# Performance work log

Hardware: AMD Instinct MI355X
Metric: run time of the kernel (lower is better)

Reference implementation:

```python
import jax, jax.numpy as jnp
import numpy as np

DIM = 384
NH = 16
HD = DIM // NH          # 24
HID = DIM * 4           # titan/cms hidden
RD = 2 * (HD // 3 // 2) # 8 rope channels per axis (d/h/w), 3*RD == HD


def _ln(x, scale, bias):
    m = x.mean(-1, keepdims=True)
    v = ((x - m) ** 2).mean(-1, keepdims=True)
    return (x - m) * jax.lax.rsqrt(v + 1e-5) * scale + bias


def _mlp(x, w1, b1, w2, b2):
    # TitanMemory / CMS level: Linear -> GELU -> Linear (titan_layers=2)
    h = jax.nn.gelu(x @ w1 + b1, approximate=False)
    return h @ w2 + b2


def _rotate(x, pos):
    # rotate_queries_or_keys: interleaved rotary. x: [B,nh,N,d], pos: [N]
    d = x.shape[-1]
    inv_freq = 1.0 / (10000.0 ** (jnp.arange(0, d, 2, dtype=jnp.float32) / d))
    ang = pos[:, None] * inv_freq[None, :]              # [N, d/2]
    sin, cos = jnp.sin(ang), jnp.cos(ang)
    x1, x2 = x[..., 0::2], x[..., 1::2]
    y1 = x1 * cos - x2 * sin
    y2 = x1 * sin + x2 * cos
    return jnp.stack([y1, y2], axis=-1).reshape(x.shape)


def _rope3d(q, T, H, W):
    # 3D RoPE on frame tokens (action_tokens=0): time / height / width axes
    B, N, D = q.shape
    qh = q.reshape(B, N, NH, HD).transpose(0, 2, 1, 3)   # [B,nh,N,hd]
    ids = jnp.arange(T * H * W)
    tpos = (ids // (H * W)).astype(jnp.float32)
    hpos = ((ids % (H * W)) // W).astype(jnp.float32)
    wpos = (ids % W).astype(jnp.float32)
    qd = _rotate(qh[..., :RD], tpos)
    qhh = _rotate(qh[..., RD:2 * RD], hpos)
    qww = _rotate(qh[..., 2 * RD:3 * RD], wpos)
    out = jnp.concatenate([qd, qhh, qww], axis=-1)
    return out.transpose(0, 2, 1, 3).reshape(B, N, D)


def setup_inputs() -> dict:
    key = jax.random.key(0)
    ks = jax.random.split(key, 8)
    B, T, H, W = 8, 8, 16, 16
    N = T * H * W
    p = lambda k, sh: jax.random.normal(k, sh, jnp.float32) * 0.02
    return {
        "x": jax.random.normal(ks[0], (B, N, DIM), jnp.float32),
        "norm1_scale": jnp.ones((DIM,), jnp.float32),
        "norm1_bias": jnp.zeros((DIM,), jnp.float32),
        "norm2_scale": jnp.ones((DIM,), jnp.float32),
        "norm2_bias": jnp.zeros((DIM,), jnp.float32),
        "q_w": p(ks[1], (DIM, DIM)),
        # stacked Titan memories: [M_k, M_v, M_eta, M_alpha, M_memory]
        "titan_w1": p(ks[2], (5, DIM, HID)),
        "titan_b1": jnp.zeros((5, HID), jnp.float32),
        "titan_w2": p(ks[3], (5, HID, DIM)),
        "titan_b2": jnp.zeros((5, DIM), jnp.float32),
        "out_w": p(ks[4], (DIM, DIM)),
        "out_b": jnp.zeros((DIM,), jnp.float32),
        # CMS levels: [fast, medium, slow]
        "cms_w1": p(ks[5], (3, DIM, HID)),
        "cms_b1": jnp.zeros((3, HID), jnp.float32),
        "cms_w2": p(ks[6], (3, HID, DIM)),
        "cms_b2": jnp.zeros((3, DIM), jnp.float32),
        "T": T, "H": H, "W": W, "action_tokens": 0,
    }


def reference(x, norm1_scale, norm1_bias, norm2_scale, norm2_bias, q_w,
              titan_w1, titan_b1, titan_w2, titan_b2, out_w, out_b,
              cms_w1, cms_b1, cms_w2, cms_b2, T, H, W, action_tokens):
    # Phase A: self-modifying Titan (eval path: retrieval only)
    y = _ln(x, norm1_scale, norm1_bias)
    q = y @ q_w                                  # static query projection (Eq. 76)
    q = _rope3d(q, T, H, W)                      # 3D RoPE (action_tokens == 0)
    out = _mlp(q, titan_w1[4], titan_b1[4], titan_w2[4], titan_b2[4])  # M_memory(q)
    out = out @ out_w + out_b                    # out_proj
    x = x + out                                  # residual (drop_path = identity)
    # Phase B: CMS multi-frequency MLP cascade
    y = _ln(x, norm2_scale, norm2_bias)
    cms = sum(_mlp(y, cms_w1[i], cms_b1[i], cms_w2[i], cms_b2[i]) for i in range(3))
    return x + cms
```

## Files before the change

kernel.cpp:

```cpp
#include <hip/hip_runtime.h>
#include <math.h>

typedef unsigned short u16;
typedef unsigned int u32;
typedef __attribute__((ext_vector_type(8))) short short8;
typedef __attribute__((ext_vector_type(4))) float f32x4;

#define DIM 384
#define HID 1536

static __device__ __forceinline__ float bf2f(u32 b){ return __uint_as_float(b << 16); }
static __device__ __forceinline__ u16 f2bf(float f){
  u32 u = __float_as_uint(f);
  u32 r = (u + 0x7fffu + ((u >> 16) & 1u)) >> 16;
  return (u16)r;
}
static __device__ __forceinline__ float gelu_fast(float v){
  float u = v * fmaf(0.0713548162726f, v * v, 1.59576912161f);
  float e = __builtin_amdgcn_exp2f(-1.44269504089f * u);
  return v * __builtin_amdgcn_rcpf(1.0f + e);
}
static __device__ __forceinline__ void gload_lds16(const u16* g, u16* l){
  __builtin_amdgcn_global_load_lds(
      (__attribute__((address_space(1))) void*)(void*)const_cast<u16*>(g),
      (__attribute__((address_space(3))) void*)(void*)l, 16, 0, 0);
}
template<int N> static __device__ __forceinline__ void vm_wait(){
  if constexpr (N == 0)      asm volatile("s_waitcnt vmcnt(0)" ::: "memory");
  else if constexpr (N == 4) asm volatile("s_waitcnt vmcnt(4)" ::: "memory");
  else if constexpr (N == 5) asm volatile("s_waitcnt vmcnt(5)" ::: "memory");
  else if constexpr (N == 6) asm volatile("s_waitcnt vmcnt(6)" ::: "memory");
  else                       asm volatile("s_waitcnt vmcnt(0)" ::: "memory");
}
static __device__ __forceinline__ void barrier_raw(){
  asm volatile("s_barrier" ::: "memory");
}
static __device__ __forceinline__ void lgkm_wait0(){
  asm volatile("s_waitcnt lgkmcnt(0)" ::: "memory");
}

__global__ __launch_bounds__(256) void ln_kernel(const float* __restrict__ x,
    const float* __restrict__ sc, const float* __restrict__ bi, u16* __restrict__ y){
  int lane = threadIdx.x & 63;
  int row = blockIdx.x * 4 + (threadIdx.x >> 6);
  const float* xr = x + (size_t)row * DIM;
  float v[6];
  float s = 0.f, sq = 0.f;
#pragma unroll
  for (int i = 0; i < 6; ++i){
    float f = xr[lane + 64*i];
    v[i] = f; s += f; sq += f*f;
  }
#pragma unroll
  for (int o = 1; o < 64; o <<= 1){ s += __shfl_xor(s, o); sq += __shfl_xor(sq, o); }
  float mean = s * (1.0f/DIM);
  float var = sq * (1.0f/DIM) - mean*mean;
  float inv = rsqrtf(var + 1e-5f);
  u16* yr = y + (size_t)row * DIM;
#pragma unroll
  for (int i = 0; i < 6; ++i){
    int c = lane + 64*i;
    yr[c] = f2bf((v[i] - mean) * inv * sc[c] + bi[c]);
  }
}

__global__ __launch_bounds__(256) void rope_kernel(u16* __restrict__ q,
    const int* __restrict__ Tp, const int* __restrict__ Hp, const int* __restrict__ Wp,
    int Mtok){
  int idx = blockIdx.x * 256 + threadIdx.x;
  int tok = idx / 192;
  if (tok >= Mtok) return;
  int p = idx - tok * 192;
  int H = *Hp, W = *Wp, T = *Tp;
  int HW = H * W;
  int Ns = T * HW;
  int n = tok % Ns;
  int head = p / 12;
  int pp = p - head * 12;
  int s = pp >> 2, f = pp & 3;
  float pos;
  if (s == 0)      pos = (float)(n / HW);
  else if (s == 1) pos = (float)((n / W) % H);
  else             pos = (float)(n % W);
  const float LOG2_10000 = 13.28771237954945f;
  float inv = __builtin_amdgcn_exp2f(-0.25f * (float)f * LOG2_10000);
  float ang = pos * inv;
  float sn = __sinf(ang), cs = __cosf(ang);
  size_t base = (size_t)tok * DIM + head * 24 + s * 8 + 2 * f;
  u32 u = *(u32*)(q + base);
  float x1 = bf2f(u & 0xffffu), x2 = bf2f(u >> 16);
  float y1 = x1 * cs - x2 * sn;
  float y2 = x1 * sn + x2 * cs;
  *(u32*)(q + base) = (u32)f2bf(y1) | ((u32)f2bf(y2) << 16);
}

template<int R, int C>
__global__ __launch_bounds__(256) void transpose_kernel(
    const float* __restrict__ s0, const float* __restrict__ s1,
    const float* __restrict__ s2, const float* __restrict__ s3,
    u16* __restrict__ d0, u16* __restrict__ d1, u16* __restrict__ d2, u16* __restrict__ d3,
    int dstStride){
  const float* src = (blockIdx.z == 0) ? s0 : (blockIdx.z == 1) ? s1 : (blockIdx.z == 2) ? s2 : s3;
  u16* dst         = (blockIdx.z == 0) ? d0 : (blockIdx.z == 1) ? d1 : (blockIdx.z == 2) ? d2 : d3;
  __shared__ u16 t[32][33];
  int tx = threadIdx.x & 31, ty = threadIdx.x >> 5;
  int r0 = blockIdx.y * 32, c0 = blockIdx.x * 32;
#pragma unroll
  for (int i = 0; i < 4; ++i)
    t[ty + 8*i][tx] = f2bf(src[(size_t)(r0 + ty + 8*i) * C + c0 + tx]);
  __syncthreads();
#pragma unroll
  for (int i = 0; i < 4; ++i)
    dst[(size_t)(c0 + ty + 8*i) * dstStride + r0 + tx] = t[tx][ty + 8*i];
}

__global__ void bias3_kernel(const float* __restrict__ b, float* __restrict__ o){
  int n = threadIdx.x;
  o[n] = b[n] + b[384 + n] + b[768 + n];
}

enum { E_NONE = 0, E_BIAS = 1, E_RES_F32 = 3, E_FINAL = 5 };

template<int BM, int N, int K, int EPI>
__global__ __launch_bounds__(256) void gemm_kernel(
    const u16* __restrict__ A, const u16* __restrict__ Bt,
    void* __restrict__ Cv, const float* __restrict__ bias,
    const float* __restrict__ res, float* __restrict__ accbuf){
  constexpr int BN = 128, BK = 64;
  constexpr int MT = BM / 32, NT = 4;
  constexpr int AIT = BM / 32, BIT = 4;
  __shared__ __align__(16) u16 As[BM * BK];
  __shared__ __align__(16) u16 Bs[BN * BK];
  const int tid = threadIdx.x;
  const int lane = tid & 63;
  const int wv = tid >> 6;
  const int wm = (wv >> 1) * (BM / 2);
  const int wn = (wv & 1) * 64;
  const int quad = lane >> 4;
  const int l16 = lane & 15;
  const int rsw = l16 & 7;
  const size_t m0 = (size_t)blockIdx.x * BM;
  const int n0 = blockIdx.y * BN;
  const int srow = lane >> 3;
  const int scol = ((lane & 7) ^ srow) * 8;

  f32x4 acc[MT][NT];
  const f32x4 zero = {0.f, 0.f, 0.f, 0.f};
#pragma unroll
  for (int mt = 0; mt < MT; ++mt)
#pragma unroll
    for (int nt = 0; nt < NT; ++nt) acc[mt][nt] = zero;

  for (int kt = 0; kt < K; kt += BK){
#pragma unroll
    for (int i = 0; i < AIT; ++i){
      int seg = i * 4 + wv;
      gload_lds16(A + (m0 + (size_t)(seg * 8 + srow)) * K + kt + scol, As + seg * 512);
    }
#pragma unroll
    for (int i = 0; i < BIT; ++i){
      int seg = i * 4 + wv;
      gload_lds16(Bt + (size_t)(n0 + seg * 8 + srow) * K + kt + scol, Bs + seg * 512);
    }
    __syncthreads();
#pragma unroll
    for (int kk = 0; kk < 2; ++kk){
      short8 af[MT], bfr[NT];
#pragma unroll
      for (int mt = 0; mt < MT; ++mt)
        af[mt] = *(const short8*)(As + (wm + mt*16 + l16) * BK + (((kk*4 + quad) ^ rsw) << 3));
#pragma unroll
      for (int nt = 0; nt < NT; ++nt)
        bfr[nt] = *(const short8*)(Bs + (wn + nt*16 + l16) * BK + (((kk*4 + quad) ^ rsw) << 3));
#pragma unroll
      for (int mt = 0; mt < MT; ++mt)
#pragma unroll
        for (int nt = 0; nt < NT; ++nt)
          acc[mt][nt] = __builtin_amdgcn_mfma_f32_16x16x32_bf16(af[mt], bfr[nt], acc[mt][nt], 0, 0, 0);
    }
    __syncthreads();
  }

#pragma unroll
  for (int mt = 0; mt < MT; ++mt){
#pragma unroll
    for (int nt = 0; nt < NT; ++nt){
      int ncol = n0 + wn + nt*16 + l16;
      float bv = (EPI != E_NONE) ? bias[ncol] : 0.f;
      size_t mbase = m0 + wm + mt*16 + quad*4;
#pragma unroll
      for (int r = 0; r < 4; ++r){
        size_t off = (mbase + r) * N + ncol;
        float vv = acc[mt][nt][r];
        if      (EPI == E_NONE)      ((u16*)Cv)[off] = f2bf(vv);
        else if (EPI == E_BIAS)      ((u16*)Cv)[off] = f2bf(vv + bv);
        else          accbuf[off] = vv + bv + res[off];
      }
    }
  }
}

template<int HIDT, int NCH, int EPI>
__global__ __launch_bounds__(512, 2) void fused_mlp4_kernel(
    const u16* __restrict__ A, const u16* __restrict__ W1t, const u16* __restrict__ W2t,
    const float* __restrict__ b1, const float* __restrict__ b2,
    const float* __restrict__ accbuf, void* __restrict__ outp){
  __shared__ __align__(16) u16 As[6 * 64 * 64];
  __shared__ __align__(16) u16 ring[2][256 * 64];
  __shared__ __align__(16) u16 Hs[4 * 64 * 64];

  const int tid  = threadIdx.x;
  const int lane = tid & 63;
  const int wv   = tid >> 6;
  const int quad = lane >> 4;
  const int l16  = lane & 15;
  const int rsw  = l16 & 7;
  const size_t m0 = (size_t)blockIdx.x * 64;
  const int srow = lane >> 3;
  const int scol = ((lane & 7) ^ srow) * 8;
  const int uwm = (wv & 1) * 32;
  const int pan = wv >> 1;
  const int dwn = wv * 48;

  auto stage_up = [&](int hc, int kt, u16* buf){
#pragma unroll
    for (int i = 0; i < 4; ++i){
      int rg = i * 8 + wv;
      gload_lds16(W1t + ((size_t)hc + rg * 8 + srow) * 384 + kt * 64 + scol,
                  buf + rg * 512);
    }
  };

#pragma unroll
  for (int i = 0; i < 6; ++i)
    gload_lds16(A + (m0 + (size_t)(wv * 8 + srow)) * 384 + i * 64 + scol,
                As + (i * 8 + wv) * 512);
  stage_up(0, 0, ring[0]);

  f32x4 cacc[4][3];
  const f32x4 zero = {0.f, 0.f, 0.f, 0.f};
#pragma unroll
  for (int mt = 0; mt < 4; ++mt)
#pragma unroll
    for (int nt = 0; nt < 3; ++nt) cacc[mt][nt] = zero;

  for (int c = 0; c < NCH; ++c){
    const int hc = c * 256;
    f32x4 hacc[2][4];
#pragma unroll
    for (int mt = 0; mt < 2; ++mt)
#pragma unroll
      for (int nt = 0; nt < 4; ++nt) hacc[mt][nt] = zero;

#pragma unroll
    for (int kt = 0; kt < 6; ++kt){
      if (kt < 5)           { stage_up(hc, kt + 1, ring[(kt + 1) & 1]); vm_wait<4>(); }
      else if (c + 1 < NCH) { stage_up(hc + 256, 0, ring[0]);           vm_wait<4>(); }
      else                  { vm_wait<0>(); }
      barrier_raw();
      const u16* buf = ring[kt & 1];
#pragma unroll
      for (int kk = 0; kk < 2; ++kk){
        short8 af[2], bfr[4];
#pragma unroll
        for (int mt = 0; mt < 2; ++mt)
          af[mt] = *(const short8*)(As + kt*4096 + (uwm + mt*16 + l16) * 64 + (((kk*4 + quad) ^ rsw) << 3));
#pragma unroll
        for (int nt = 0; nt < 4; ++nt)
          bfr[nt] = *(const short8*)(buf + (pan*64 + nt*16 + l16) * 64 + (((kk*4 + quad) ^ rsw) << 3));
#pragma unroll
        for (int mt = 0; mt < 2; ++mt)
#pragma unroll
          for (int nt = 0; nt < 4; ++nt)
            hacc[mt][nt] = __builtin_amdgcn_mfma_f32_16x16x32_bf16(af[mt], bfr[nt], hacc[mt][nt], 0, 0, 0);
      }
      barrier_raw();
    }

#pragma unroll
    for (int nt = 0; nt < 4; ++nt){
      int pc = nt*16 + l16;
      float bv = b1[hc + pan*64 + pc];
      u16* hp = Hs + pan*4096;
#pragma unroll
      for (int mt = 0; mt < 2; ++mt){
#pragma unroll
        for (int r = 0; r < 4; ++r){
          int row = uwm + mt*16 + quad*4 + r;
          hp[row*64 + (((pc >> 3) ^ (row & 7)) << 3) + (pc & 7)] = f2bf(gelu_fast(hacc[mt][nt][r] + bv));
        }
      }
    }
    lgkm_wait0();
    barrier_raw();

    short8 wb[2][3];
#pragma unroll
    for (int nt = 0; nt < 3; ++nt)
      wb[0][nt] = *(const short8*)(W2t + (size_t)(dwn + nt*16 + l16) * HIDT + hc + quad*8);
#pragma unroll
    for (int s = 0; s < 8; ++s){
      if (s < 7){
        int off = ((s+1) >> 1) * 64 + (((s+1) & 1) * 4 + quad) * 8;
#pragma unroll
        for (int nt = 0; nt < 3; ++nt)
          wb[(s+1) & 1][nt] = *(const short8*)(W2t + (size_t)(dwn + nt*16 + l16) * HIDT + hc + off);
      }
      int dt = s >> 1, kk = s & 1;
      short8 af[4];
#pragma unroll
      for (int mt = 0; mt < 4; ++mt)
        af[mt] = *(const short8*)(Hs + dt*4096 + (mt*16 + l16) * 64 + (((kk*4 + quad) ^ rsw) << 3));
#pragma unroll
      for (int mt = 0; mt < 4; ++mt)
#pragma unroll
        for (int nt = 0; nt < 3; ++nt)
          cacc[mt][nt] = __builtin_amdgcn_mfma_f32_16x16x32_bf16(af[mt], wb[s & 1][nt], cacc[mt][nt], 0, 0, 0);
    }
  }

#pragma unroll
  for (int nt = 0; nt < 3; ++nt){
    int col = dwn + nt*16 + l16;
    float bv = b2[col];
#pragma unroll
    for (int mt = 0; mt < 4; ++mt){
      size_t mbase = m0 + mt*16 + quad*4;
#pragma unroll
      for (int r = 0; r < 4; ++r){
        size_t off = (mbase + r) * DIM + col;
        float vv = cacc[mt][nt][r] + bv;
        if (EPI == E_BIAS) ((u16*)outp)[off] = f2bf(vv);
        else  ((float*)outp)[off] = accbuf[off] + vv;
      }
    }
  }
}

extern "C" void kernel_launch(void* const* d_in, const int* in_sizes, int n_in,
                              void* d_out, int out_size, void* d_ws, size_t ws_size,
                              hipStream_t stream) {
  const int W11 = DIM * HID;
  const float* x   = (const float*)d_in[0];
  const float* n1s = (const float*)d_in[1];
  const float* n1b = (const float*)d_in[2];
  const float* n2s = (const float*)d_in[3];
  const float* n2b = (const float*)d_in[4];
  const float* qw  = (const float*)d_in[5];
  const float* tw1 = (const float*)d_in[6] + 4 * W11;
  const float* tb1 = (const float*)d_in[7] + 4 * HID;
  const float* tw2 = (const float*)d_in[8] + 4 * W11;
  const float* tb2 = (const float*)d_in[9] + 4 * DIM;
  const float* ow  = (const float*)d_in[10];
  const float* ob  = (const float*)d_in[11];
  const float* cw1 = (const float*)d_in[12];
  const float* cb1 = (const float*)d_in[13];
  const float* cw2 = (const float*)d_in[14];
  const float* cb2 = (const float*)d_in[15];
  const int* Tp = (const int*)d_in[16];
  const int* Hp = (const int*)d_in[17];
  const int* Wp = (const int*)d_in[18];
  const int M = in_sizes[0] / DIM;

  char* ws = (char*)d_ws;
  if (ws_size < 22611456u) return;
  u16*  y    = (u16*) (ws + 0);
  u16*  qwT  = (u16*) (ws + 12582912);
  u16*  owT  = (u16*) (ws + 12877824);
  u16*  w1T  = (u16*) (ws + 13172736);
  u16*  w2T  = (u16*) (ws + 14352384);
  u16*  cw1T = (u16*) (ws + 15532032);
  u16*  cw2T = (u16*) (ws + 19070976);
  float* cb2s = (float*)(ws + 22609920);
  u16*  qb   = (u16*)d_out;

  transpose_kernel<384,384><<<dim3(12,12,2),256,0,stream>>>(
      qw, ow, qw, qw, qwT, owT, qwT, qwT, 384);
  transpose_kernel<384,1536><<<dim3(48,12,4),256,0,stream>>>(
      tw1, cw1, cw1 + W11, cw1 + 2*W11, w1T, cw1T, cw1T + W11, cw1T + 2*W11, 384);
  transpose_kernel<1536,384><<<dim3(12,48,1),256,0,stream>>>(
      tw2, tw2, tw2, tw2, w2T, w2T, w2T, w2T, 1536);
  transpose_kernel<1536,384><<<dim3(12,48,3),256,0,stream>>>(
      cw2, cw2 + W11, cw2 + 2*W11, cw2, cw2T, cw2T + 1536, cw2T + 3072, cw2T, 4608);
  bias3_kernel<<<1,384,0,stream>>>(cb2, cb2s);

  ln_kernel<<<M/4,256,0,stream>>>(x, n1s, n1b, y);
  gemm_kernel<64,384,384,E_NONE><<<dim3(M/64,3),256,0,stream>>>(y, qwT, qb, nullptr, nullptr, nullptr);
  rope_kernel<<<(M*192)/256,256,0,stream>>>(qb, Tp, Hp, Wp, M);
  fused_mlp4_kernel<1536,6,E_BIAS><<<M/64,512,0,stream>>>(
      qb, w1T, w2T, tb1, tb2, nullptr, y);
  gemm_kernel<64,384,384,E_RES_F32><<<dim3(M/64,3),256,0,stream>>>(
      y, owT, nullptr, ob, x, (float*)d_out);
  ln_kernel<<<M/4,256,0,stream>>>((const float*)d_out, n2s, n2b, y);
  fused_mlp4_kernel<4608,18,E_FINAL><<<M/64,512,0,stream>>>(
      y, cw1T, cw2T, cb1, cb2s, (const float*)d_out, d_out);
}
```

Baseline: 450.8 us.

## Halve fused MLP row tile to 32 and drop double-buffered W1 staging

The fused MLP kernel now processes 32 rows per block instead of 64, doubling the grid and shrinking LDS so more blocks can be resident (launch bounds raised to 4 blocks per CU). The double-buffered W1 ring with manual vmcnt waits is replaced by a single staging buffer loaded each k-step and guarded by __syncthreads. The aim is more occupancy and parallelism, but each block now streams the same weights for half as many rows, doubling weight traffic. Weight-load latency is also no longer overlapped with compute inside a block.

```diff
diff --git a/kernel.cpp b/kernel.cpp
--- a/kernel.cpp
+++ b/kernel.cpp
@@ -24,19 +24,6 @@
   __builtin_amdgcn_global_load_lds(
       (__attribute__((address_space(1))) void*)(void*)const_cast<u16*>(g),
       (__attribute__((address_space(3))) void*)(void*)l, 16, 0, 0);
-}
-template<int N> static __device__ __forceinline__ void vm_wait(){
-  if constexpr (N == 0)      asm volatile("s_waitcnt vmcnt(0)" ::: "memory");
-  else if constexpr (N == 4) asm volatile("s_waitcnt vmcnt(4)" ::: "memory");
-  else if constexpr (N == 5) asm volatile("s_waitcnt vmcnt(5)" ::: "memory");
-  else if constexpr (N == 6) asm volatile("s_waitcnt vmcnt(6)" ::: "memory");
-  else                       asm volatile("s_waitcnt vmcnt(0)" ::: "memory");
-}
-static __device__ __forceinline__ void barrier_raw(){
-  asm volatile("s_barrier" ::: "memory");
-}
-static __device__ __forceinline__ void lgkm_wait0(){
-  asm volatile("s_waitcnt lgkmcnt(0)" ::: "memory");
 }
 
 __global__ __launch_bounds__(256) void ln_kernel(const float* __restrict__ x,
@@ -201,13 +188,13 @@
 }
 
 template<int HIDT, int NCH, int EPI>
-__global__ __launch_bounds__(512, 2) void fused_mlp4_kernel(
+__global__ __launch_bounds__(512, 4) void fused_mlp5_kernel(
     const u16* __restrict__ A, const u16* __restrict__ W1t, const u16* __restrict__ W2t,
     const float* __restrict__ b1, const float* __restrict__ b2,
     const float* __restrict__ accbuf, void* __restrict__ outp){
-  __shared__ __align__(16) u16 As[6 * 64 * 64];
-  __shared__ __align__(16) u16 ring[2][256 * 64];
-  __shared__ __align__(16) u16 Hs[4 * 64 * 64];
+  __shared__ __align__(16) u16 As[6 * 32 * 64];
+  __shared__ __align__(16) u16 WB[256 * 64];
+  __shared__ __align__(16) u16 Hs[4 * 32 * 64];
 
   const int tid  = threadIdx.x;
   const int lane = tid & 63;
@@ -215,84 +202,77 @@
   const int quad = lane >> 4;
   const int l16  = lane & 15;
   const int rsw  = l16 & 7;
-  const size_t m0 = (size_t)blockIdx.x * 64;
+  const size_t m0 = (size_t)blockIdx.x * 32;
   const int srow = lane >> 3;
   const int scol = ((lane & 7) ^ srow) * 8;
-  const int uwm = (wv & 1) * 32;
-  const int pan = wv >> 1;
+  const int pan = wv;
   const int dwn = wv * 48;
 
-  auto stage_up = [&](int hc, int kt, u16* buf){
-#pragma unroll
-    for (int i = 0; i < 4; ++i){
-      int rg = i * 8 + wv;
-      gload_lds16(W1t + ((size_t)hc + rg * 8 + srow) * 384 + kt * 64 + scol,
-                  buf + rg * 512);
-    }
-  };
-
-#pragma unroll
-  for (int i = 0; i < 6; ++i)
-    gload_lds16(A + (m0 + (size_t)(wv * 8 + srow)) * 384 + i * 64 + scol,
-                As + (i * 8 + wv) * 512);
-  stage_up(0, 0, ring[0]);
-
-  f32x4 cacc[4][3];
+#pragma unroll
+  for (int i = 0; i < 3; ++i){
+    int g = wv * 3 + i;
+    gload_lds16(A + (m0 + (size_t)((g & 3) * 8 + srow)) * 384 + (g >> 2) * 64 + scol,
+                As + g * 512);
+  }
+
+  f32x4 cacc[2][3];
   const f32x4 zero = {0.f, 0.f, 0.f, 0.f};
 #pragma unroll
-  for (int mt = 0; mt < 4; ++mt)
+  for (int mt = 0; mt < 2; ++mt)
 #pragma unroll
     for (int nt = 0; nt < 3; ++nt) cacc[mt][nt] = zero;
 
   for (int c = 0; c < NCH; ++c){
     const int hc = c * 256;
-    f32x4 hacc[2][4];
+    f32x4 hacc[2][2];
 #pragma unroll
     for (int mt = 0; mt < 2; ++mt)
 #pragma unroll
-      for (int nt = 0; nt < 4; ++nt) hacc[mt][nt] = zero;
-
-#pragma unroll
+      for (int nt = 0; nt < 2; ++nt) hacc[mt][nt] = zero;
+
     for (int kt = 0; kt < 6; ++kt){
-      if (kt < 5)           { stage_up(hc, kt + 1, ring[(kt + 1) & 1]); vm_wait<4>(); }
-      else if (c + 1 < NCH) { stage_up(hc + 256, 0, ring[0]);           vm_wait<4>(); }
-      else                  { vm_wait<0>(); }
-      barrier_raw();
-      const u16* buf = ring[kt & 1];
+#pragma unroll
+      for (int i = 0; i < 4; ++i){
+        int g = i * 8 + wv;
+        gload_lds16(W1t + ((size_t)hc + g * 8 + srow) * 384 + kt * 64 + scol,
+                    WB + g * 512);
+      }
+      __syncthreads();
 #pragma unroll
       for (int kk = 0; kk < 2; ++kk){
-        short8 af[2], bfr[4];
+        short8 af[2], bfr[2];
 #pragma unroll
         for (int mt = 0; mt < 2; ++mt)
-          af[mt] = *(const short8*)(As + kt*4096 + (uwm + mt*16 + l16) * 64 + (((kk*4 + quad) ^ rsw) << 3));
-#pragma unroll
-        for (int nt = 0; nt < 4; ++nt)
-          bfr[nt] = *(const short8*)(buf + (pan*64 + nt*16 + l16) * 64 + (((kk*4 + quad) ^ rsw) << 3));
+          af[mt] = *(const short8*)(As + kt*2048 + (mt*16 + l16) * 64 + (((kk*4 + quad) ^ rsw) << 3));
+#pragma unroll
+        for (int nt = 0; nt < 2; ++nt)
+          bfr[nt] = *(const short8*)(WB + (pan*32 + nt*16 + l16) * 64 + (((kk*4 + quad) ^ rsw) << 3));
 #pragma unroll
         for (int mt = 0; mt < 2; ++mt)
 #pragma unroll
-          for (int nt = 0; nt < 4; ++nt)
+          for (int nt = 0; nt < 2; ++nt)
             hacc[mt][nt] = __builtin_amdgcn_mfma_f32_16x16x32_bf16(af[mt], bfr[nt], hacc[mt][nt], 0, 0, 0);
       }
-      barrier_raw();
-    }
-
-#pragma unroll
-    for (int nt = 0; nt < 4; ++nt){
+      __syncthreads();
+    }
+
+#pragma unroll
+    for (int nt = 0; nt < 2; ++nt){
       int pc = nt*16 + l16;
-      float bv = b1[hc + pan*64 + pc];
-      u16* hp = Hs + pan*4096;
+      int hcol = pan*32 + pc;
+      float bv = b1[hc + hcol];
+      u16* hp = Hs + (hcol >> 6) * 2048;
+      int cw = hcol & 63;
 #pragma unroll
       for (int mt = 0; mt < 2; ++mt){
 #pragma unroll
         for (int r = 0; r < 4; ++r){
-          int row = uwm + mt*16 + quad*4 + r;
-          hp[row*64 + (((pc >> 3) ^ (row & 7)) << 3) + (pc & 7)] = f2bf(gelu_fast(hacc[mt][nt][r] + bv));
+          int row = mt*16 + quad*4 + r;
+          hp[row*64 + (((cw >> 3) ^ (row & 7)) << 3) + (cw & 7)] = f2bf(gelu_fast(hacc[mt][nt][r] + bv));
         }
       }
     }
-    lgkm_wait0();
-    barrier_raw();
+    __syncthreads();
 
     short8 wb[2][3];
 #pragma unroll
@@ -307,16 +287,17 @@
           wb[(s+1) & 1][nt] = *(const short8*)(W2t + (size_t)(dwn + nt*16 + l16) * HIDT + hc + off);
       }
       int dt = s >> 1, kk = s & 1;
-      short8 af[4];
-#pragma unroll
-      for (int mt = 0; mt < 4; ++mt)
-        af[mt] = *(const short8*)(Hs + dt*4096 + (mt*16 + l16) * 64 + (((kk*4 + quad) ^ rsw) << 3));
-#pragma unroll
-      for (int mt = 0; mt < 4; ++mt)
+      short8 af[2];
+#pragma unroll
+      for (int mt = 0; mt < 2; ++mt)
+        af[mt] = *(const short8*)(Hs + dt*2048 + (mt*16 + l16) * 64 + (((kk*4 + quad) ^ rsw) << 3));
+#pragma unroll
+      for (int mt = 0; mt < 2; ++mt)
 #pragma unroll
         for (int nt = 0; nt < 3; ++nt)
           cacc[mt][nt] = __builtin_amdgcn_mfma_f32_16x16x32_bf16(af[mt], wb[s & 1][nt], cacc[mt][nt], 0, 0, 0);
     }
+    __syncthreads();
   }
 
 #pragma unroll
@@ -324,7 +305,7 @@
     int col = dwn + nt*16 + l16;
     float bv = b2[col];
 #pragma unroll
-    for (int mt = 0; mt < 4; ++mt){
+    for (int mt = 0; mt < 2; ++mt){
       size_t mbase = m0 + mt*16 + quad*4;
 #pragma unroll
       for (int r = 0; r < 4; ++r){
@@ -387,11 +368,11 @@
   ln_kernel<<<M/4,256,0,stream>>>(x, n1s, n1b, y);
   gemm_kernel<64,384,384,E_NONE><<<dim3(M/64,3),256,0,stream>>>(y, qwT, qb, nullptr, nullptr, nullptr);
   rope_kernel<<<(M*192)/256,256,0,stream>>>(qb, Tp, Hp, Wp, M);
-  fused_mlp4_kernel<1536,6,E_BIAS><<<M/64,512,0,stream>>>(
+  fused_mlp5_kernel<1536,6,E_BIAS><<<M/32,512,0,stream>>>(
       qb, w1T, w2T, tb1, tb2, nullptr, y);
   gemm_kernel<64,384,384,E_RES_F32><<<dim3(M/64,3),256,0,stream>>>(
       y, owT, nullptr, ob, x, (float*)d_out);
   ln_kernel<<<M/4,256,0,stream>>>((const float*)d_out, n2s, n2b, y);
-  fused_mlp4_kernel<4608,18,E_FINAL><<<M/64,512,0,stream>>>(
+  fused_mlp5_kernel<4608,18,E_FINAL><<<M/32,512,0,stream>>>(
       y, cw1T, cw2T, cb1, cb2s, (const float*)d_out, d_out);
 }
```

Measured after the change: 580.9 us. 28.8% more time.
